# Kernel tuning notes

Hardware: AMD Instinct MI355X
Metric: run time of the kernel (lower is better)

Reference implementation:

```python
import jax, jax.numpy as jnp
import numpy as np

B, CIN, H, W = 2, 192, 56, 56
ODIM, HEADS, K, PAD, STRIDE = 192, 6, 7, 3, 1


def setup_inputs() -> dict:
    key = jax.random.key(0)
    ks = jax.random.split(key, 6)
    w_scale = 0.02
    return {
        "x": jax.random.normal(ks[0], (B, CIN, H, W), dtype=jnp.float32),
        "wq": jax.random.normal(ks[1], (ODIM, CIN), dtype=jnp.float32) * w_scale,
        "wk": jax.random.normal(ks[2], (ODIM, CIN), dtype=jnp.float32) * w_scale,
        "wv": jax.random.normal(ks[3], (ODIM, CIN), dtype=jnp.float32) * w_scale,
        "pos_embedding": jax.random.normal(ks[4], (1, 2 * K - 1), dtype=jnp.float32),
        "w_proj": jax.random.normal(ks[5], (ODIM, ODIM), dtype=jnp.float32) * w_scale,
        "kernel_size": K,
        "padding": PAD,
        "stride": STRIDE,
        "num_heads": HEADS,
    }


def _patches(x, k, pad, stride):
    # torch.nn.Unfold(kernel_size=k, padding=pad, stride=stride), kept as
    # (B, C, k*k, oh, ow) with window offsets ordered row-major (i*k + j),
    # channel slowest -- matching torch's (C, kh, kw) flattening.
    xp = jnp.pad(x, ((0, 0), (0, 0), (pad, pad), (pad, pad)))
    Hp, Wp = xp.shape[2], xp.shape[3]
    oh = (Hp - k) // stride + 1
    ow = (Wp - k) // stride + 1
    sl = [xp[:, :, i:i + stride * (oh - 1) + 1:stride, j:j + stride * (ow - 1) + 1:stride]
          for i in range(k) for j in range(k)]
    return jnp.stack(sl, axis=2)


def reference(x, wq, wk, wv, pos_embedding, w_proj, kernel_size, padding, stride, num_heads):
    b, c, h, w = x.shape
    # 1x1 convs (no bias) == channel matmuls
    q = jnp.einsum('oc,bchw->bohw', wq, x)
    k = jnp.einsum('oc,bchw->bohw', wk, x)
    v = jnp.einsum('oc,bchw->bohw', wv, x)
    # Unfold(kernel=1, stride=s) on q == strided spatial subsampling
    q = q[:, :, ::stride, ::stride]
    kp = _patches(k, kernel_size, padding, stride)  # (B, O, K*K, oh, ow)
    vp = _patches(v, kernel_size, padding, stride)
    oh, ow = kp.shape[3], kp.shape[4]
    d = wq.shape[0] // num_heads
    kk = kernel_size * kernel_size
    qh = q.reshape(b, num_heads, d, oh, ow)
    kh = kp.reshape(b, num_heads, d, kk, oh, ow)
    vh = vp.reshape(b, num_heads, d, kk, oh, ow)
    # per-pixel windowed attention scores: (B, heads, K*K, oh, ow)
    attn = jnp.einsum('bhdij,bhdkij->bhkij', qh, kh)
    # relative position bias: index = row_offset + col_offset (0 .. 2K-2)
    coords = np.arange(kernel_size)
    rel = (coords[:, None] + coords[None, :]).reshape(-1)  # (K*K,)
    bias = pos_embedding[0][jnp.asarray(rel)]  # (K*K,)
    attn = jax.nn.softmax(attn + bias[None, None, :, None, None], axis=2)
    out = jnp.einsum('bhkij,bhdkij->bhdij', attn, vh)
    out = out.reshape(b, num_heads * d, oh, ow)
    return jnp.einsum('oc,bchw->bohw', w_proj, out)
```

## Files before the change

kernel.cpp:

```cpp
#include <hip/hip_runtime.h>


#define HW    3136
#define WIMG  56
#define CIN   192
#define QKVLD 576
#define SMEM_BYTES 53312

using short8 = __attribute__((ext_vector_type(8))) short;
using f32x4  = __attribute__((ext_vector_type(4))) float;

__device__ __forceinline__ unsigned short f2bf(float f) {
    union { float f; unsigned u; } v; v.f = f;
    unsigned r = v.u + 0x7fffu + ((v.u >> 16) & 1u);
    return (unsigned short)(r >> 16);
}
__device__ __forceinline__ unsigned pack2(float a, float b) {
    return (unsigned)f2bf(a) | ((unsigned)f2bf(b) << 16);
}
__device__ __forceinline__ float bflo(unsigned u) {
    union { unsigned u; float f; } v; v.u = u << 16; return v.f;
}
__device__ __forceinline__ float bfhi(unsigned u) {
    union { unsigned u; float f; } v; v.u = u & 0xffff0000u; return v.f;
}
__device__ __forceinline__ float qsum4(float s) {
    union { float f; int i; } u, t;
    u.f = s;
    t.i = __builtin_amdgcn_update_dpp(0, u.i, 0xB1, 0xF, 0xF, true);
    u.f += t.f;
    t.i = __builtin_amdgcn_update_dpp(0, u.i, 0x4E, 0xF, 0xF, true);
    u.f += t.f;
    return u.f;
}

__global__ __launch_bounds__(256) void k_p1(
    const float* __restrict__ x, const float* __restrict__ wq,
    const float* __restrict__ wk, const float* __restrict__ wv,
    unsigned short* __restrict__ qkv)
{
    extern __shared__ char smem[];
    unsigned short* As  = (unsigned short*)smem;
    unsigned short* Bs  = As + 64 * 200;
    unsigned*       Asw = (unsigned*)smem;
    unsigned*       Bsw = (unsigned*)(smem + 25600);

    const int tid = threadIdx.x;
    const int lane = tid & 63, wave = tid >> 6;
    const int l15  = lane & 15, quad = lane >> 4;
    const int wm   = (wave & 1) * 32, wn = (wave >> 1) * 32;

    const int t = blockIdx.x;
    const int mt = t % 98, nt = t / 98;
    const int m0 = mt * 64, n0 = nt * 64;
    const float* Wp = (nt < 3) ? (wq + (size_t)n0 * CIN)
                    : (nt < 6) ? (wk + (size_t)(n0 - 192) * CIN)
                               : (wv + (size_t)(n0 - 384) * CIN);

    #pragma unroll
    for (int i = 0; i < 6; ++i) {
        int u = tid + 256 * i;
        int pq = u & 15, c2 = u >> 4;
        int pp = m0 + pq * 4;
        int bb = (pp >= HW) ? 1 : 0;
        const float* src = x + ((size_t)(bb * CIN + c2 * 2)) * HW + (pp - bb * HW);
        float4 f0 = *(const float4*)src;
        float4 f1 = *(const float4*)(src + HW);
        Asw[(pq * 4 + 0) * 100 + c2] = pack2(f0.x, f1.x);
        Asw[(pq * 4 + 1) * 100 + c2] = pack2(f0.y, f1.y);
        Asw[(pq * 4 + 2) * 100 + c2] = pack2(f0.z, f1.z);
        Asw[(pq * 4 + 3) * 100 + c2] = pack2(f0.w, f1.w);
    }
    {
        int o = tid >> 2, c4 = tid & 3;
        #pragma unroll
        for (int i = 0; i < 12; ++i) {
            int cq = c4 + 4 * i;
            float4 w = *(const float4*)(Wp + (size_t)o * CIN + cq * 4);
            uint2 d; d.x = pack2(w.x, w.y); d.y = pack2(w.z, w.w);
            *(uint2*)(Bsw + o * 100 + cq * 2) = d;
        }
    }
    __syncthreads();

    f32x4 acc[2][2] = {};
    const unsigned short* pa0 = As + (wm + l15) * 200 + quad * 8;
    const unsigned short* pb0 = Bs + (wn + l15) * 200 + quad * 8;
    #pragma unroll
    for (int s = 0; s < 6; ++s) {
        short8 a0 = *(const short8*)(pa0 + s * 32);
        short8 a1 = *(const short8*)(pa0 + 16 * 200 + s * 32);
        short8 b0 = *(const short8*)(pb0 + s * 32);
        short8 b1 = *(const short8*)(pb0 + 16 * 200 + s * 32);
        acc[0][0] = __builtin_amdgcn_mfma_f32_16x16x32_bf16(a0, b0, acc[0][0], 0, 0, 0);
        acc[0][1] = __builtin_amdgcn_mfma_f32_16x16x32_bf16(a0, b1, acc[0][1], 0, 0, 0);
        acc[1][0] = __builtin_amdgcn_mfma_f32_16x16x32_bf16(a1, b0, acc[1][0], 0, 0, 0);
        acc[1][1] = __builtin_amdgcn_mfma_f32_16x16x32_bf16(a1, b1, acc[1][1], 0, 0, 0);
    }

    const int gm = m0 + wm + quad * 4;
    const int gn = n0 + wn + l15;
    #pragma unroll
    for (int ti = 0; ti < 2; ++ti)
        #pragma unroll
        for (int tj = 0; tj < 2; ++tj)
            #pragma unroll
            for (int rr = 0; rr < 4; ++rr)
                qkv[(size_t)(gm + ti * 16 + rr) * QKVLD + (gn + tj * 16)] =
                    f2bf(acc[ti][tj][rr]);
}

__global__ __launch_bounds__(256) void k_p2(
    const unsigned short* __restrict__ qkv, const float* __restrict__ pos,
    unsigned short* __restrict__ oact)
{
    extern __shared__ char smem[];
    float* kbuf = (float*)smem;
    float* vbuf = kbuf + 6664;

    const int tid = threadIdx.x;
    const int t = blockIdx.x;
    const int tz = t / 49, r49 = t - tz * 49;
    const int ty = r49 / 7, tx = r49 - ty * 7;
    const int bq = tz / 6, h = tz - bq * 6;
    const int y0 = ty * 8 - 3, x0 = tx * 8 - 3;

    #pragma unroll
    for (int i = 0; i < 7; ++i) {
        int u = tid + 256 * i;
        if (u < 1568) {
            int pp = u >> 3, uu = u & 7;
            int part = uu >> 2, sub8 = uu & 3;
            int py = pp / 14, px = pp - py * 14;
            int gy = y0 + py, gx = x0 + px;
            float f0=0,f1=0,f2=0,f3=0,f4=0,f5=0,f6=0,f7=0;
            if ((unsigned)gy < 56u && (unsigned)gx < 56u) {
                uint4 rv = *(const uint4*)(qkv +
                    (size_t)(bq * HW + gy * WIMG + gx) * QKVLD +
                    192 + part * 192 + h * 32 + sub8 * 8);
                f0=bflo(rv.x); f1=bfhi(rv.x); f2=bflo(rv.y); f3=bfhi(rv.y);
                f4=bflo(rv.z); f5=bfhi(rv.z); f6=bflo(rv.w); f7=bfhi(rv.w);
            }
            float* dst = (part ? vbuf : kbuf) + pp * 34 + sub8 * 8;
            *(float2*)(dst + 0) = make_float2(f0, f1);
            *(float2*)(dst + 2) = make_float2(f2, f3);
            *(float2*)(dst + 4) = make_float2(f4, f5);
            *(float2*)(dst + 6) = make_float2(f6, f7);
        }
    }
    __syncthreads();

    const int sub = tid & 3, pix = tid >> 2;
    const int py = pix >> 3, px = pix & 7;
    const int y = ty * 8 + py, xx = tx * 8 + px;
    const int p = y * WIMG + xx;

    uint4 qv = *(const uint4*)(qkv + (size_t)(bq * HW + p) * QKVLD + h * 32 + sub * 8);
    float q0=bflo(qv.x), q1=bfhi(qv.x), q2=bflo(qv.y), q3=bfhi(qv.y);
    float q4=bflo(qv.z), q5=bfhi(qv.z), q6=bflo(qv.w), q7=bfhi(qv.w);

    float posr[13];
    #pragma unroll
    for (int i = 0; i < 13; ++i) posr[i] = pos[i];

    float logits[49];
    #pragma unroll
    for (int kk = 0; kk < 49; ++kk) {
        const int ky = kk / 7, kx = kk % 7;
        const int pp = (py + ky) * 14 + (px + kx);
        const float2* kp = (const float2*)(kbuf + pp * 34 + sub * 8);
        float2 k0 = kp[0], k1 = kp[1], k2 = kp[2], k3 = kp[3];
        float s = 0.f;
        s = fmaf(q0, k0.x, s); s = fmaf(q1, k0.y, s);
        s = fmaf(q2, k1.x, s); s = fmaf(q3, k1.y, s);
        s = fmaf(q4, k2.x, s); s = fmaf(q5, k2.y, s);
        s = fmaf(q6, k3.x, s); s = fmaf(q7, k3.y, s);
        logits[kk] = qsum4(s) + posr[ky + kx];
    }

    float m = logits[0];
    #pragma unroll
    for (int kk = 1; kk < 49; ++kk) m = fmaxf(m, logits[kk]);
    float sum = 0.f;
    #pragma unroll
    for (int kk = 0; kk < 49; ++kk) {
        logits[kk] = __expf(logits[kk] - m);
        sum += logits[kk];
    }

    float a0=0,a1=0,a2=0,a3=0,a4=0,a5=0,a6=0,a7=0;
    #pragma unroll
    for (int kk = 0; kk < 49; ++kk) {
        const int ky = kk / 7, kx = kk % 7;
        const int pp = (py + ky) * 14 + (px + kx);
        const float2* vp = (const float2*)(vbuf + pp * 34 + sub * 8);
        float2 v0 = vp[0], v1 = vp[1], v2 = vp[2], v3 = vp[3];
        const float pw = logits[kk];
        a0 = fmaf(pw, v0.x, a0); a1 = fmaf(pw, v0.y, a1);
        a2 = fmaf(pw, v1.x, a2); a3 = fmaf(pw, v1.y, a3);
        a4 = fmaf(pw, v2.x, a4); a5 = fmaf(pw, v2.y, a5);
        a6 = fmaf(pw, v3.x, a6); a7 = fmaf(pw, v3.y, a7);
    }
    const float inv = 1.f / sum;
    a0 *= inv; a1 *= inv; a2 *= inv; a3 *= inv;
    a4 *= inv; a5 *= inv; a6 *= inv; a7 *= inv;

    ushort4 h0, h1;
    h0.x = f2bf(a0); h0.y = f2bf(a1); h0.z = f2bf(a2); h0.w = f2bf(a3);
    h1.x = f2bf(a4); h1.y = f2bf(a5); h1.z = f2bf(a6); h1.w = f2bf(a7);
    unsigned short* ob = oact + (size_t)(bq * HW + p) * CIN + h * 32 + sub * 8;
    *(ushort4*)ob       = h0;
    *(ushort4*)(ob + 4) = h1;
}

__global__ __launch_bounds__(256) void k_p3(
    const float* __restrict__ wproj, const unsigned short* __restrict__ oact,
    float* __restrict__ out)
{
    extern __shared__ char smem[];
    unsigned short* As  = (unsigned short*)smem;
    unsigned short* Bs  = As + 64 * 200;
    unsigned*       Asw = (unsigned*)smem;

    const int tid = threadIdx.x;
    const int lane = tid & 63, wave = tid >> 6;
    const int l15  = lane & 15, quad = lane >> 4;
    const int wm   = (wave & 1) * 32, wn = (wave >> 1) * 32;

    const int t = blockIdx.x;
    const int mt = t % 3, pt = t / 3;
    {
        int o = tid >> 2, c4 = tid & 3;
        #pragma unroll
        for (int i = 0; i < 12; ++i) {
            int cq = c4 + 4 * i;
            float4 w = *(const float4*)(wproj + (size_t)(mt * 64 + o) * CIN + cq * 4);
            uint2 d; d.x = pack2(w.x, w.y); d.y = pack2(w.z, w.w);
            *(uint2*)(Asw + o * 100 + cq * 2) = d;
        }
    }
    {
        int rw = tid >> 2, s4 = tid & 3;
        #pragma unroll
        for (int i = 0; i < 6; ++i) {
            int seg = s4 + 4 * i;
            uint4 dv = *(const uint4*)(oact + (size_t)(pt * 64 + rw) * CIN + seg * 8);
            *(uint4*)(Bs + rw * 200 + seg * 8) = dv;
        }
    }
    __syncthreads();

    f32x4 acc[2][2] = {};
    const unsigned short* pa0 = As + (wm + l15) * 200 + quad * 8;
    const unsigned short* pb0 = Bs + (wn + l15) * 200 + quad * 8;
    #pragma unroll
    for (int s = 0; s < 6; ++s) {
        short8 a0 = *(const short8*)(pa0 + s * 32);
        short8 a1 = *(const short8*)(pa0 + 16 * 200 + s * 32);
        short8 b0 = *(const short8*)(pb0 + s * 32);
        short8 b1 = *(const short8*)(pb0 + 16 * 200 + s * 32);
        acc[0][0] = __builtin_amdgcn_mfma_f32_16x16x32_bf16(a0, b0, acc[0][0], 0, 0, 0);
        acc[0][1] = __builtin_amdgcn_mfma_f32_16x16x32_bf16(a0, b1, acc[0][1], 0, 0, 0);
        acc[1][0] = __builtin_amdgcn_mfma_f32_16x16x32_bf16(a1, b0, acc[1][0], 0, 0, 0);
        acc[1][1] = __builtin_amdgcn_mfma_f32_16x16x32_bf16(a1, b1, acc[1][1], 0, 0, 0);
    }

    const int bb = (pt * 64 >= HW) ? 1 : 0;
    const int pl = pt * 64 - bb * HW + wn + l15;
    const int go = mt * 64 + wm + quad * 4;
    float* Yb = out + (size_t)bb * (CIN * HW);
    #pragma unroll
    for (int ti = 0; ti < 2; ++ti)
        #pragma unroll
        for (int tj = 0; tj < 2; ++tj)
            #pragma unroll
            for (int rr = 0; rr < 4; ++rr)
                Yb[(size_t)(go + ti * 16 + rr) * HW + pl + tj * 16] = acc[ti][tj][rr];
}

extern "C" void kernel_launch(void* const* d_in, const int* in_sizes, int n_in,
                              void* d_out, int out_size, void* d_ws, size_t ws_size,
                              hipStream_t stream)
{
    const float* x     = (const float*)d_in[0];
    const float* wq    = (const float*)d_in[1];
    const float* wk    = (const float*)d_in[2];
    const float* wv    = (const float*)d_in[3];
    const float* pos   = (const float*)d_in[4];
    const float* wproj = (const float*)d_in[5];

    char* ws = (char*)d_ws;
    unsigned short* qkvp  = (unsigned short*)ws;
    unsigned short* oactp = (unsigned short*)(ws + 7225344);
    float*          outp  = (float*)d_out;

    k_p1<<<dim3(882), dim3(256), SMEM_BYTES, stream>>>(x, wq, wk, wv, qkvp);
    k_p2<<<dim3(588), dim3(256), SMEM_BYTES, stream>>>(qkvp, pos, oactp);
    k_p3<<<dim3(294), dim3(256), SMEM_BYTES, stream>>>(wproj, oactp, outp);
}
```

Baseline: 105.6 us.

## Process two adjacent pixels per thread in windowed attention with online softmax

The attention kernel now uses 128 threads per block, and each thread handles two horizontally adjacent pixels. Per window row it loads 8 K/V columns once and shares them between the two pixels, and it switches to a row-wise online softmax so the 49 logits no longer need to be kept in registers. It also uses hardware packed bf16 conversion in the QKV epilogue and in the output stores. The intent is to cut LDS traffic per output. The cost is more registers per thread, half as many threads per block, and extra exp rescaling work.

```diff
diff --git a/kernel.cpp b/kernel.cpp
--- a/kernel.cpp
+++ b/kernel.cpp
@@ -16,7 +16,9 @@
     return (unsigned short)(r >> 16);
 }
 __device__ __forceinline__ unsigned pack2(float a, float b) {
-    return (unsigned)f2bf(a) | ((unsigned)f2bf(b) << 16);
+    unsigned r;
+    asm("v_cvt_pk_bf16_f32 %0, %1, %2" : "=v"(r) : "v"(a), "v"(b));
+    return r;
 }
 __device__ __forceinline__ float bflo(unsigned u) {
     union { unsigned u; float f; } v; v.u = u << 16; return v.f;
@@ -105,12 +107,16 @@
         #pragma unroll
         for (int tj = 0; tj < 2; ++tj)
             #pragma unroll
-            for (int rr = 0; rr < 4; ++rr)
+            for (int rr = 0; rr < 4; rr += 2) {
+                unsigned r = pack2(acc[ti][tj][rr], acc[ti][tj][rr + 1]);
                 qkv[(size_t)(gm + ti * 16 + rr) * QKVLD + (gn + tj * 16)] =
-                    f2bf(acc[ti][tj][rr]);
-}
-
-__global__ __launch_bounds__(256) void k_p2(
+                    (unsigned short)r;
+                qkv[(size_t)(gm + ti * 16 + rr + 1) * QKVLD + (gn + tj * 16)] =
+                    (unsigned short)(r >> 16);
+            }
+}
+
+__global__ __launch_bounds__(128) void k_p2(
     const unsigned short* __restrict__ qkv, const float* __restrict__ pos,
     unsigned short* __restrict__ oact)
 {
@@ -125,14 +131,25 @@
     const int bq = tz / 6, h = tz - bq * 6;
     const int y0 = ty * 8 - 3, x0 = tx * 8 - 3;
 
-    #pragma unroll
-    for (int i = 0; i < 7; ++i) {
-        int u = tid + 256 * i;
+    const int sub = tid & 3, pix2 = tid >> 2;
+    const int py = pix2 >> 2, pxA = (pix2 & 3) * 2;
+    const int y = ty * 8 + py, xA = tx * 8 + pxA;
+    const int pA = y * WIMG + xA;
+
+    uint4 qva = *(const uint4*)(qkv + (size_t)(bq * HW + pA) * QKVLD + h * 32 + sub * 8);
+    uint4 qvb = *(const uint4*)(qkv + (size_t)(bq * HW + pA + 1) * QKVLD + h * 32 + sub * 8);
+    float posr[13];
+    #pragma unroll
+    for (int i = 0; i < 13; ++i) posr[i] = pos[i];
+
+    #pragma unroll
+    for (int i = 0; i < 13; ++i) {
+        int u = tid + 128 * i;
         if (u < 1568) {
             int pp = u >> 3, uu = u & 7;
             int part = uu >> 2, sub8 = uu & 3;
-            int py = pp / 14, px = pp - py * 14;
-            int gy = y0 + py, gx = x0 + px;
+            int ppy = pp / 14, ppx = pp - ppy * 14;
+            int gy = y0 + ppy, gx = x0 + ppx;
             float f0=0,f1=0,f2=0,f3=0,f4=0,f5=0,f6=0,f7=0;
             if ((unsigned)gy < 56u && (unsigned)gx < 56u) {
                 uint4 rv = *(const uint4*)(qkv +
@@ -150,67 +167,95 @@
     }
     __syncthreads();
 
-    const int sub = tid & 3, pix = tid >> 2;
-    const int py = pix >> 3, px = pix & 7;
-    const int y = ty * 8 + py, xx = tx * 8 + px;
-    const int p = y * WIMG + xx;
-
-    uint4 qv = *(const uint4*)(qkv + (size_t)(bq * HW + p) * QKVLD + h * 32 + sub * 8);
-    float q0=bflo(qv.x), q1=bfhi(qv.x), q2=bflo(qv.y), q3=bfhi(qv.y);
-    float q4=bflo(qv.z), q5=bfhi(qv.z), q6=bflo(qv.w), q7=bfhi(qv.w);
-
-    float posr[13];
-    #pragma unroll
-    for (int i = 0; i < 13; ++i) posr[i] = pos[i];
-
-    float logits[49];
-    #pragma unroll
-    for (int kk = 0; kk < 49; ++kk) {
-        const int ky = kk / 7, kx = kk % 7;
-        const int pp = (py + ky) * 14 + (px + kx);
-        const float2* kp = (const float2*)(kbuf + pp * 34 + sub * 8);
-        float2 k0 = kp[0], k1 = kp[1], k2 = kp[2], k3 = kp[3];
-        float s = 0.f;
-        s = fmaf(q0, k0.x, s); s = fmaf(q1, k0.y, s);
-        s = fmaf(q2, k1.x, s); s = fmaf(q3, k1.y, s);
-        s = fmaf(q4, k2.x, s); s = fmaf(q5, k2.y, s);
-        s = fmaf(q6, k3.x, s); s = fmaf(q7, k3.y, s);
-        logits[kk] = qsum4(s) + posr[ky + kx];
-    }
-
-    float m = logits[0];
-    #pragma unroll
-    for (int kk = 1; kk < 49; ++kk) m = fmaxf(m, logits[kk]);
-    float sum = 0.f;
-    #pragma unroll
-    for (int kk = 0; kk < 49; ++kk) {
-        logits[kk] = __expf(logits[kk] - m);
-        sum += logits[kk];
-    }
-
-    float a0=0,a1=0,a2=0,a3=0,a4=0,a5=0,a6=0,a7=0;
-    #pragma unroll
-    for (int kk = 0; kk < 49; ++kk) {
-        const int ky = kk / 7, kx = kk % 7;
-        const int pp = (py + ky) * 14 + (px + kx);
-        const float2* vp = (const float2*)(vbuf + pp * 34 + sub * 8);
-        float2 v0 = vp[0], v1 = vp[1], v2 = vp[2], v3 = vp[3];
-        const float pw = logits[kk];
-        a0 = fmaf(pw, v0.x, a0); a1 = fmaf(pw, v0.y, a1);
-        a2 = fmaf(pw, v1.x, a2); a3 = fmaf(pw, v1.y, a3);
-        a4 = fmaf(pw, v2.x, a4); a5 = fmaf(pw, v2.y, a5);
-        a6 = fmaf(pw, v3.x, a6); a7 = fmaf(pw, v3.y, a7);
-    }
-    const float inv = 1.f / sum;
-    a0 *= inv; a1 *= inv; a2 *= inv; a3 *= inv;
-    a4 *= inv; a5 *= inv; a6 *= inv; a7 *= inv;
-
-    ushort4 h0, h1;
-    h0.x = f2bf(a0); h0.y = f2bf(a1); h0.z = f2bf(a2); h0.w = f2bf(a3);
-    h1.x = f2bf(a4); h1.y = f2bf(a5); h1.z = f2bf(a6); h1.w = f2bf(a7);
-    unsigned short* ob = oact + (size_t)(bq * HW + p) * CIN + h * 32 + sub * 8;
-    *(ushort4*)ob       = h0;
-    *(ushort4*)(ob + 4) = h1;
+    float qa[8], qb[8];
+    qa[0]=bflo(qva.x); qa[1]=bfhi(qva.x); qa[2]=bflo(qva.y); qa[3]=bfhi(qva.y);
+    qa[4]=bflo(qva.z); qa[5]=bfhi(qva.z); qa[6]=bflo(qva.w); qa[7]=bfhi(qva.w);
+    qb[0]=bflo(qvb.x); qb[1]=bfhi(qvb.x); qb[2]=bflo(qvb.y); qb[3]=bfhi(qvb.y);
+    qb[4]=bflo(qvb.z); qb[5]=bfhi(qvb.z); qb[6]=bflo(qvb.w); qb[7]=bfhi(qvb.w);
+
+    float accA[8] = {0,0,0,0,0,0,0,0}, accB[8] = {0,0,0,0,0,0,0,0};
+    float mA = -1e30f, mB = -1e30f, sA = 0.f, sB = 0.f;
+
+    #pragma unroll
+    for (int ky = 0; ky < 7; ++ky) {
+        const int rowo = ((py + ky) * 14 + pxA) * 34 + sub * 8;
+        const float* rk = kbuf + rowo;
+        float dA[7], dB[7];
+        #pragma unroll
+        for (int c = 0; c < 8; ++c) {
+            const float2* cp = (const float2*)(rk + c * 34);
+            float2 c0 = cp[0], c1 = cp[1], c2 = cp[2], c3 = cp[3];
+            if (c < 7) {
+                float s = 0.f;
+                s = fmaf(qa[0], c0.x, s); s = fmaf(qa[1], c0.y, s);
+                s = fmaf(qa[2], c1.x, s); s = fmaf(qa[3], c1.y, s);
+                s = fmaf(qa[4], c2.x, s); s = fmaf(qa[5], c2.y, s);
+                s = fmaf(qa[6], c3.x, s); s = fmaf(qa[7], c3.y, s);
+                dA[c] = s;
+            }
+            if (c > 0) {
+                float s = 0.f;
+                s = fmaf(qb[0], c0.x, s); s = fmaf(qb[1], c0.y, s);
+                s = fmaf(qb[2], c1.x, s); s = fmaf(qb[3], c1.y, s);
+                s = fmaf(qb[4], c2.x, s); s = fmaf(qb[5], c2.y, s);
+                s = fmaf(qb[6], c3.x, s); s = fmaf(qb[7], c3.y, s);
+                dB[c - 1] = s;
+            }
+        }
+        float lA[7], lB[7];
+        #pragma unroll
+        for (int c = 0; c < 7; ++c) {
+            lA[c] = qsum4(dA[c]) + posr[ky + c];
+            lB[c] = qsum4(dB[c]) + posr[ky + c];
+        }
+        float mAn = mA, mBn = mB;
+        #pragma unroll
+        for (int c = 0; c < 7; ++c) { mAn = fmaxf(mAn, lA[c]); mBn = fmaxf(mBn, lB[c]); }
+        const float scA = __expf(mA - mAn), scB = __expf(mB - mBn);
+        mA = mAn; mB = mBn;
+        sA *= scA; sB *= scB;
+        float pwA[7], pwB[7];
+        #pragma unroll
+        for (int c = 0; c < 7; ++c) {
+            pwA[c] = __expf(lA[c] - mA); sA += pwA[c];
+            pwB[c] = __expf(lB[c] - mB); sB += pwB[c];
+        }
+        #pragma unroll
+        for (int j = 0; j < 8; ++j) { accA[j] *= scA; accB[j] *= scB; }
+        const float* rv = vbuf + rowo;
+        #pragma unroll
+        for (int c = 0; c < 8; ++c) {
+            const float2* vp = (const float2*)(rv + c * 34);
+            float2 v0 = vp[0], v1 = vp[1], v2 = vp[2], v3 = vp[3];
+            if (c < 7) {
+                const float w = pwA[c];
+                accA[0]=fmaf(w,v0.x,accA[0]); accA[1]=fmaf(w,v0.y,accA[1]);
+                accA[2]=fmaf(w,v1.x,accA[2]); accA[3]=fmaf(w,v1.y,accA[3]);
+                accA[4]=fmaf(w,v2.x,accA[4]); accA[5]=fmaf(w,v2.y,accA[5]);
+                accA[6]=fmaf(w,v3.x,accA[6]); accA[7]=fmaf(w,v3.y,accA[7]);
+            }
+            if (c > 0) {
+                const float w = pwB[c - 1];
+                accB[0]=fmaf(w,v0.x,accB[0]); accB[1]=fmaf(w,v0.y,accB[1]);
+                accB[2]=fmaf(w,v1.x,accB[2]); accB[3]=fmaf(w,v1.y,accB[3]);
+                accB[4]=fmaf(w,v2.x,accB[4]); accB[5]=fmaf(w,v2.y,accB[5]);
+                accB[6]=fmaf(w,v3.x,accB[6]); accB[7]=fmaf(w,v3.y,accB[7]);
+            }
+        }
+    }
+
+    const float invA = 1.f / sA, invB = 1.f / sB;
+    uint4 oA, oB;
+    oA.x = pack2(accA[0]*invA, accA[1]*invA);
+    oA.y = pack2(accA[2]*invA, accA[3]*invA);
+    oA.z = pack2(accA[4]*invA, accA[5]*invA);
+    oA.w = pack2(accA[6]*invA, accA[7]*invA);
+    oB.x = pack2(accB[0]*invB, accB[1]*invB);
+    oB.y = pack2(accB[2]*invB, accB[3]*invB);
+    oB.z = pack2(accB[4]*invB, accB[5]*invB);
+    oB.w = pack2(accB[6]*invB, accB[7]*invB);
+    *(uint4*)(oact + (size_t)(bq * HW + pA) * CIN + h * 32 + sub * 8)     = oA;
+    *(uint4*)(oact + (size_t)(bq * HW + pA + 1) * CIN + h * 32 + sub * 8) = oB;
 }
 
 __global__ __launch_bounds__(256) void k_p3(
@@ -295,6 +340,6 @@
     float*          outp  = (float*)d_out;
 
     k_p1<<<dim3(882), dim3(256), SMEM_BYTES, stream>>>(x, wq, wk, wv, qkvp);
-    k_p2<<<dim3(588), dim3(256), SMEM_BYTES, stream>>>(qkvp, pos, oactp);
+    k_p2<<<dim3(588), dim3(128), SMEM_BYTES, stream>>>(qkvp, pos, oactp);
     k_p3<<<dim3(294), dim3(256), SMEM_BYTES, stream>>>(wproj, oactp, outp);
 }
```

Result: slower. 119.6 us (+13.2%).
